# Kernel tuning notes

Measured on AMD Instinct MI355X. Metric: run time of the kernel, lower is better.

## Reference

```python
import jax, jax.numpy as jnp
import numpy as np


def setup_inputs() -> dict:
    key = jax.random.key(0)
    k1, k2 = jax.random.split(key)
    q_embed = jax.random.normal(k1, (1000, 1024), dtype=jnp.float32)      # (V, D)
    conv_feat = jax.random.normal(k2, (64, 1024, 800), dtype=jnp.float32)  # (B, D, T)
    return {"q_embed": q_embed, "conv_feat": conv_feat}


def reference(q_embed, conv_feat):
    # sim_scores: (B, V, T) = q_embed (V, D) @ conv_feat (B, D, T), no scaling
    sim_scores = jnp.einsum('vd,bdt->bvt', q_embed, conv_feat)
    attention_weights = jax.nn.softmax(sim_scores, axis=2)  # over T
    # context: (B, V, D) = weights (B, V, T) @ conv_feat^T (B, T, D)
    context_vector = jnp.einsum('bvt,bdt->bvd', attention_weights, conv_feat)
    return (context_vector, attention_weights)
```

## Files before the change

### kernel.cpp

```cpp
#include <hip/hip_runtime.h>
#include <hip/hip_bf16.h>

typedef short bf16x8 __attribute__((ext_vector_type(8)));
typedef float f32x4 __attribute__((ext_vector_type(4)));

#define NV 1000
#define ND 1024
#define NT 800
#define NB 64

__device__ inline unsigned short f32_bf16(float f) {
    unsigned u = __builtin_bit_cast(unsigned, f);
    return (unsigned short)((u + 0x7FFFu + ((u >> 16) & 1u)) >> 16);
}
__device__ inline void split_bf16(float f, unsigned short& h, unsigned short& l) {
    unsigned u = __builtin_bit_cast(unsigned, f);
    unsigned hb = (u + 0x7FFFu + ((u >> 16) & 1u)) >> 16;
    h = (unsigned short)hb;
    float hf = __builtin_bit_cast(float, hb << 16);
    float lf = f - hf;
    unsigned ul = __builtin_bit_cast(unsigned, lf);
    l = (unsigned short)((ul + 0x7FFFu + ((ul >> 16) & 1u)) >> 16);
}

__device__ inline void gload16(const void* g, void* l) {
    __builtin_amdgcn_global_load_lds(
        (const __attribute__((address_space(1))) unsigned int*)g,
        (__attribute__((address_space(3))) unsigned int*)l, 16, 0, 0);
}

__global__ __launch_bounds__(256) void prep_q(const float* __restrict__ Q,
                                              unsigned short* __restrict__ Qh,
                                              unsigned short* __restrict__ Ql) {
    int idx = blockIdx.x * 256 + threadIdx.x;
    int row = idx >> 8;
    int c4 = (idx & 255) << 2;
    float4 f = make_float4(0.f, 0.f, 0.f, 0.f);
    if (row < NV) f = *(const float4*)(Q + (size_t)row * ND + c4);
    unsigned short h0,h1,h2,h3,l0,l1,l2,l3;
    split_bf16(f.x,h0,l0); split_bf16(f.y,h1,l1);
    split_bf16(f.z,h2,l2); split_bf16(f.w,h3,l3);
    *(ushort4*)(Qh + (size_t)row * ND + c4) = make_ushort4(h0,h1,h2,h3);
    *(ushort4*)(Ql + (size_t)row * ND + c4) = make_ushort4(l0,l1,l2,l3);
}

__global__ __launch_bounds__(256) void prep_c(const float* __restrict__ C,
                                              unsigned short* __restrict__ Cth,
                                              unsigned short* __restrict__ Ctl) {
    const int dt = blockIdx.x;
    const int tt = blockIdx.y;
    const int b  = blockIdx.z;
    const int tid = threadIdx.x;
    __shared__ float T[64][33];
    const float* Cb = C + (size_t)b * ND * NT;
    const int d0 = dt * 64, t0 = tt * 32;
#pragma unroll
    for (int r = 0; r < 2; ++r) {
        int idx = r * 256 + tid;
        int row = idx >> 3;
        int c4 = (idx & 7) << 2;
        float4 f = *(const float4*)(Cb + (size_t)(d0 + row) * NT + t0 + c4);
        T[row][c4 + 0] = f.x; T[row][c4 + 1] = f.y;
        T[row][c4 + 2] = f.z; T[row][c4 + 3] = f.w;
    }
    __syncthreads();
#pragma unroll
    for (int r = 0; r < 2; ++r) {
        int idx = r * 256 + tid;
        int trow = idx >> 4;
        int dc = (idx & 15) << 2;
        unsigned short h[4], l[4];
#pragma unroll
        for (int j = 0; j < 4; ++j) split_bf16(T[dc + j][trow], h[j], l[j]);
        size_t o = ((size_t)b * NT + t0 + trow) * ND + d0 + dc;
        *(ushort4*)(Cth + o) = make_ushort4(h[0],h[1],h[2],h[3]);
        *(ushort4*)(Ctl + o) = make_ushort4(l[0],l[1],l[2],l[3]);
    }
}

__global__ __launch_bounds__(256) void gemm1_kernel(const unsigned short* __restrict__ Qh,
                                                    const unsigned short* __restrict__ Ql,
                                                    const unsigned short* __restrict__ Cth,
                                                    const unsigned short* __restrict__ Ctl,
                                                    float* __restrict__ S) {
    const int h = blockIdx.x;
    const int L = (h & 7) * 320 + (h >> 3);
    const int bm = L & 7;
    const int rest = L >> 3;
    const int bn = rest % 5;
    const int b  = rest / 5;

    const int tid = threadIdx.x;
    const int lane = tid & 63;
    const int w = tid >> 6;
    const int wr = w >> 1, wc = w & 1;

    __shared__ unsigned short Ah[128 * 32];
    __shared__ unsigned short Al[128 * 32];
    __shared__ unsigned short Bh[160 * 32];
    __shared__ unsigned short Bl[160 * 32];

    const int v0 = bm * 128, t0 = bn * 160;
    const unsigned short* Agh = Qh + (size_t)v0 * ND;
    const unsigned short* Agl = Ql + (size_t)v0 * ND;
    const unsigned short* Bgh = Cth + ((size_t)b * NT + t0) * ND;
    const unsigned short* Bgl = Ctl + ((size_t)b * NT + t0) * ND;

    f32x4 acc[4][5];
#pragma unroll
    for (int i = 0; i < 4; ++i)
#pragma unroll
        for (int j = 0; j < 5; ++j) acc[i][j] = (f32x4){0.f, 0.f, 0.f, 0.f};

    const int srow = lane >> 2;
    const int sslot = lane & 3;

    for (int k0 = 0; k0 < ND; k0 += 32) {
        for (int i = w; i < 8; i += 4) {
            int row = i * 16 + srow;
            int c = ((sslot ^ (row & 3)) << 3) + k0;
            gload16(Agh + (size_t)row * ND + c, Ah + i * 512);
            gload16(Agl + (size_t)row * ND + c, Al + i * 512);
        }
        for (int i = w; i < 10; i += 4) {
            int row = i * 16 + srow;
            int c = ((sslot ^ (row & 3)) << 3) + k0;
            gload16(Bgh + (size_t)row * ND + c, Bh + i * 512);
            gload16(Bgl + (size_t)row * ND + c, Bl + i * 512);
        }
        __syncthreads();

        const int g = lane >> 4, rl = lane & 15;
        const int sx = (g ^ (rl & 3)) << 4;
        bf16x8 ah[4], al[4], bh[5], bl[5];
#pragma unroll
        for (int mf = 0; mf < 4; ++mf) {
            int off = (wr * 64 + mf * 16 + rl) * 64 + sx;
            ah[mf] = *(const bf16x8*)((const char*)Ah + off);
            al[mf] = *(const bf16x8*)((const char*)Al + off);
        }
#pragma unroll
        for (int nf = 0; nf < 5; ++nf) {
            int off = (wc * 80 + nf * 16 + rl) * 64 + sx;
            bh[nf] = *(const bf16x8*)((const char*)Bh + off);
            bl[nf] = *(const bf16x8*)((const char*)Bl + off);
        }
#pragma unroll
        for (int mf = 0; mf < 4; ++mf)
#pragma unroll
            for (int nf = 0; nf < 5; ++nf) {
                acc[mf][nf] = __builtin_amdgcn_mfma_f32_16x16x32_bf16(ah[mf], bh[nf], acc[mf][nf], 0, 0, 0);
                acc[mf][nf] = __builtin_amdgcn_mfma_f32_16x16x32_bf16(ah[mf], bl[nf], acc[mf][nf], 0, 0, 0);
                acc[mf][nf] = __builtin_amdgcn_mfma_f32_16x16x32_bf16(al[mf], bh[nf], acc[mf][nf], 0, 0, 0);
            }
        __syncthreads();
    }

    float* Sb = S + (size_t)b * NV * NT;
    const int g = lane >> 4, rl = lane & 15;
#pragma unroll
    for (int mf = 0; mf < 4; ++mf) {
#pragma unroll
        for (int nf = 0; nf < 5; ++nf) {
#pragma unroll
            for (int r = 0; r < 4; ++r) {
                int v = v0 + wr * 64 + mf * 16 + g * 4 + r;
                int t = t0 + wc * 80 + nf * 16 + rl;
                if (v < NV) Sb[(size_t)v * NT + t] = acc[mf][nf][r];
            }
        }
    }
}

__global__ __launch_bounds__(256) void softmax_kernel(float* __restrict__ S) {
    const int row = blockIdx.x * 4 + (threadIdx.x >> 6);
    const int lane = threadIdx.x & 63;
    float* p = S + (size_t)row * NT;
    float v[13];
    float m = -INFINITY;
#pragma unroll
    for (int i = 0; i < 13; ++i) {
        int t = i * 64 + lane;
        v[i] = (t < NT) ? p[t] : -INFINITY;
        m = fmaxf(m, v[i]);
    }
#pragma unroll
    for (int off = 32; off; off >>= 1) m = fmaxf(m, __shfl_xor(m, off));
    float s = 0.f;
#pragma unroll
    for (int i = 0; i < 13; ++i) {
        int t = i * 64 + lane;
        float e = (t < NT) ? __expf(v[i] - m) : 0.f;
        v[i] = e;
        s += e;
    }
#pragma unroll
    for (int off = 32; off; off >>= 1) s += __shfl_xor(s, off);
    const float inv = 1.0f / s;
#pragma unroll
    for (int i = 0; i < 13; ++i) {
        int t = i * 64 + lane;
        if (t < NT) p[t] = v[i] * inv;
    }
}

__global__ __launch_bounds__(256) void gemm2_kernel(const float* __restrict__ W,
                                                    const float* __restrict__ C,
                                                    float* __restrict__ O) {
    const int h = blockIdx.x;
    const int L = (h & 7) * 512 + (h >> 3);
    const int bm = L & 7;
    const int bn = (L >> 3) & 7;
    const int b  = L >> 6;
    const int tid = threadIdx.x;
    const int lane = tid & 63;
    const int wid = tid >> 6;
    const int wr = wid >> 1;
    const int wc = wid & 1;

    __shared__ unsigned short As[128][40];
    __shared__ unsigned short Bs[128][40];

    const float* Wb = W + (size_t)b * NV * NT;
    const float* Cb = C + (size_t)b * ND * NT;
    const int v0 = bm * 128;
    const int d0 = bn * 128;

    f32x4 acc[4][4];
#pragma unroll
    for (int i = 0; i < 4; ++i)
#pragma unroll
        for (int j = 0; j < 4; ++j) acc[i][j] = (f32x4){0.f, 0.f, 0.f, 0.f};

    for (int k0 = 0; k0 < NT; k0 += 32) {
#pragma unroll
        for (int r = 0; r < 4; ++r) {
            int idx = r * 256 + tid;
            int row = idx >> 3;
            int kq  = (idx & 7) << 2;
            int v = v0 + row; if (v > NV - 1) v = NV - 1;
            const float4 f = *(const float4*)(Wb + (size_t)v * NT + k0 + kq);
            *(ushort4*)&As[row][kq] = make_ushort4(f32_bf16(f.x), f32_bf16(f.y), f32_bf16(f.z), f32_bf16(f.w));
        }
#pragma unroll
        for (int r = 0; r < 4; ++r) {
            int idx = r * 256 + tid;
            int row = idx >> 3;
            int kq  = (idx & 7) << 2;
            const float4 f = *(const float4*)(Cb + (size_t)(d0 + row) * NT + k0 + kq);
            *(ushort4*)&Bs[row][kq] = make_ushort4(f32_bf16(f.x), f32_bf16(f.y), f32_bf16(f.z), f32_bf16(f.w));
        }
        __syncthreads();

        bf16x8 a[4], bfr[4];
        const int kk = (lane >> 4) << 3;
#pragma unroll
        for (int mf = 0; mf < 4; ++mf) {
            int row = wr * 64 + mf * 16 + (lane & 15);
            a[mf] = *(const bf16x8*)&As[row][kk];
        }
#pragma unroll
        for (int nf = 0; nf < 4; ++nf) {
            int row = wc * 64 + nf * 16 + (lane & 15);
            bfr[nf] = *(const bf16x8*)&Bs[row][kk];
        }
#pragma unroll
        for (int mf = 0; mf < 4; ++mf)
#pragma unroll
            for (int nf = 0; nf < 4; ++nf)
                acc[mf][nf] = __builtin_amdgcn_mfma_f32_16x16x32_bf16(a[mf], bfr[nf], acc[mf][nf], 0, 0, 0);
        __syncthreads();
    }

    float* Ob = O + (size_t)b * NV * ND;
#pragma unroll
    for (int mf = 0; mf < 4; ++mf) {
#pragma unroll
        for (int nf = 0; nf < 4; ++nf) {
#pragma unroll
            for (int r = 0; r < 4; ++r) {
                int v = v0 + wr * 64 + mf * 16 + (lane >> 4) * 4 + r;
                int d = d0 + wc * 64 + nf * 16 + (lane & 15);
                if (v < NV) Ob[(size_t)v * ND + d] = acc[mf][nf][r];
            }
        }
    }
}

extern "C" void kernel_launch(void* const* d_in, const int* in_sizes, int n_in,
                              void* d_out, int out_size, void* d_ws, size_t ws_size,
                              hipStream_t stream) {
    const float* Q = (const float*)d_in[0];
    const float* C = (const float*)d_in[1];
    float* ctx = (float*)d_out;
    float* wts = ctx + (size_t)NB * NV * ND;

    unsigned short* Cth = (unsigned short*)ctx;
    unsigned short* Ctl = Cth + (size_t)NB * NT * ND;
    unsigned short* Qh  = Ctl + (size_t)NB * NT * ND;
    unsigned short* Ql  = Qh + (size_t)1024 * ND;

    prep_q<<<dim3(1024), 256, 0, stream>>>(Q, Qh, Ql);
    prep_c<<<dim3(16, 25, NB), 256, 0, stream>>>(C, Cth, Ctl);
    gemm1_kernel<<<dim3(2560), 256, 0, stream>>>(Qh, Ql, Cth, Ctl, wts);
    softmax_kernel<<<dim3(16000), 256, 0, stream>>>(wts);
    gemm2_kernel<<<dim3(4096), 256, 0, stream>>>(wts, C, ctx);
}
```

Before: 798.7 us.

## Pre-convert softmax weights and conv features to bf16 for direct-load gemm2

Softmax now also writes a bf16 copy of the attention weights, and prep_c writes a bf16 copy of conv_feat in its original layout, both into workspace. A new gemm2 path loads these bf16 tiles straight into swizzled shared memory with 16-byte loads, so it no longer reads fp32 and converts inside the GEMM. There are fallback variants for when the workspace is too small. The cost is extra global writes of two large bf16 buffers in earlier kernels, and the path depends on ws_size.

Result: faster. 735.6 us (-7.9%).

```diff
diff --git a/kernel.cpp b/kernel.cpp
--- a/kernel.cpp
+++ b/kernel.cpp
@@ -46,7 +46,9 @@
 
 __global__ __launch_bounds__(256) void prep_c(const float* __restrict__ C,
                                               unsigned short* __restrict__ Cth,
-                                              unsigned short* __restrict__ Ctl) {
+                                              unsigned short* __restrict__ Ctl,
+                                              unsigned short* __restrict__ Cbf,
+                                              int writeCbf) {
     const int dt = blockIdx.x;
     const int tt = blockIdx.y;
     const int b  = blockIdx.z;
@@ -62,6 +64,10 @@
         float4 f = *(const float4*)(Cb + (size_t)(d0 + row) * NT + t0 + c4);
         T[row][c4 + 0] = f.x; T[row][c4 + 1] = f.y;
         T[row][c4 + 2] = f.z; T[row][c4 + 3] = f.w;
+        if (writeCbf) {
+            *(ushort4*)(Cbf + ((size_t)b * ND + d0 + row) * NT + t0 + c4) =
+                make_ushort4(f32_bf16(f.x), f32_bf16(f.y), f32_bf16(f.z), f32_bf16(f.w));
+        }
     }
     __syncthreads();
 #pragma unroll
@@ -172,10 +178,13 @@
     }
 }
 
-__global__ __launch_bounds__(256) void softmax_kernel(float* __restrict__ S) {
+__global__ __launch_bounds__(256) void softmax_kernel(float* __restrict__ S,
+                                                      unsigned short* __restrict__ Wbf,
+                                                      int writeWbf) {
     const int row = blockIdx.x * 4 + (threadIdx.x >> 6);
     const int lane = threadIdx.x & 63;
     float* p = S + (size_t)row * NT;
+    unsigned short* pw = Wbf + (size_t)row * NT;
     float v[13];
     float m = -INFINITY;
 #pragma unroll
@@ -200,13 +209,177 @@
 #pragma unroll
     for (int i = 0; i < 13; ++i) {
         int t = i * 64 + lane;
-        if (t < NT) p[t] = v[i] * inv;
-    }
-}
-
-__global__ __launch_bounds__(256) void gemm2_kernel(const float* __restrict__ W,
-                                                    const float* __restrict__ C,
-                                                    float* __restrict__ O) {
+        if (t < NT) {
+            float wv = v[i] * inv;
+            p[t] = wv;
+            if (writeWbf) pw[t] = f32_bf16(wv);
+        }
+    }
+}
+
+__global__ __launch_bounds__(256) void gemm2_fast(const unsigned short* __restrict__ Wbf,
+                                                  const unsigned short* __restrict__ Cbf,
+                                                  float* __restrict__ O) {
+    const int h = blockIdx.x;
+    const int L = (h & 7) * 512 + (h >> 3);
+    const int bm = L & 7;
+    const int bn = (L >> 3) & 7;
+    const int b  = L >> 6;
+    const int tid = threadIdx.x;
+    const int lane = tid & 63;
+    const int w = tid >> 6;
+    const int wr = w >> 1, wc = w & 1;
+
+    __shared__ unsigned short As[128 * 32];
+    __shared__ unsigned short Bs[128 * 32];
+
+    const int v0 = bm * 128, d0 = bn * 128;
+    const unsigned short* Ag = Wbf + (size_t)b * NV * NT;
+    const unsigned short* Bg = Cbf + ((size_t)b * ND + d0) * NT;
+
+    f32x4 acc[4][4];
+#pragma unroll
+    for (int i = 0; i < 4; ++i)
+#pragma unroll
+        for (int j = 0; j < 4; ++j) acc[i][j] = (f32x4){0.f, 0.f, 0.f, 0.f};
+
+    const int srow = lane >> 2;
+    const int sslot = lane & 3;
+
+    for (int k0 = 0; k0 < NT; k0 += 32) {
+        for (int i = w; i < 8; i += 4) {
+            int row = i * 16 + srow;
+            int c = ((sslot ^ (row & 3)) << 3) + k0;
+            int vrow = v0 + row; if (vrow > NV - 1) vrow = NV - 1;
+            gload16(Ag + (size_t)vrow * NT + c, As + i * 512);
+            gload16(Bg + (size_t)row * NT + c, Bs + i * 512);
+        }
+        __syncthreads();
+
+        const int g = lane >> 4, rl = lane & 15;
+        const int sx = (g ^ (rl & 3)) << 4;
+        bf16x8 a[4], bfr[4];
+#pragma unroll
+        for (int mf = 0; mf < 4; ++mf) {
+            int off = (wr * 64 + mf * 16 + rl) * 64 + sx;
+            a[mf] = *(const bf16x8*)((const char*)As + off);
+        }
+#pragma unroll
+        for (int nf = 0; nf < 4; ++nf) {
+            int off = (wc * 64 + nf * 16 + rl) * 64 + sx;
+            bfr[nf] = *(const bf16x8*)((const char*)Bs + off);
+        }
+#pragma unroll
+        for (int mf = 0; mf < 4; ++mf)
+#pragma unroll
+            for (int nf = 0; nf < 4; ++nf)
+                acc[mf][nf] = __builtin_amdgcn_mfma_f32_16x16x32_bf16(a[mf], bfr[nf], acc[mf][nf], 0, 0, 0);
+        __syncthreads();
+    }
+
+    float* Ob = O + (size_t)b * NV * ND;
+    const int g = lane >> 4, rl = lane & 15;
+#pragma unroll
+    for (int mf = 0; mf < 4; ++mf) {
+#pragma unroll
+        for (int nf = 0; nf < 4; ++nf) {
+#pragma unroll
+            for (int r = 0; r < 4; ++r) {
+                int v = v0 + wr * 64 + mf * 16 + g * 4 + r;
+                int d = d0 + wc * 64 + nf * 16 + rl;
+                if (v < NV) Ob[(size_t)v * ND + d] = acc[mf][nf][r];
+            }
+        }
+    }
+}
+
+__global__ __launch_bounds__(256) void gemm2_mid(const unsigned short* __restrict__ Wbf,
+                                                 const float* __restrict__ C,
+                                                 float* __restrict__ O) {
+    const int h = blockIdx.x;
+    const int L = (h & 7) * 512 + (h >> 3);
+    const int bm = L & 7;
+    const int bn = (L >> 3) & 7;
+    const int b  = L >> 6;
+    const int tid = threadIdx.x;
+    const int lane = tid & 63;
+    const int w = tid >> 6;
+    const int wr = w >> 1, wc = w & 1;
+
+    __shared__ unsigned short As[128 * 32];
+    __shared__ unsigned short Bs[128][40];
+
+    const int v0 = bm * 128, d0 = bn * 128;
+    const unsigned short* Ag = Wbf + (size_t)b * NV * NT;
+    const float* Cb = C + (size_t)b * ND * NT;
+
+    f32x4 acc[4][4];
+#pragma unroll
+    for (int i = 0; i < 4; ++i)
+#pragma unroll
+        for (int j = 0; j < 4; ++j) acc[i][j] = (f32x4){0.f, 0.f, 0.f, 0.f};
+
+    const int srow = lane >> 2;
+    const int sslot = lane & 3;
+
+    for (int k0 = 0; k0 < NT; k0 += 32) {
+        for (int i = w; i < 8; i += 4) {
+            int row = i * 16 + srow;
+            int c = ((sslot ^ (row & 3)) << 3) + k0;
+            int vrow = v0 + row; if (vrow > NV - 1) vrow = NV - 1;
+            gload16(Ag + (size_t)vrow * NT + c, As + i * 512);
+        }
+#pragma unroll
+        for (int r = 0; r < 4; ++r) {
+            int idx = r * 256 + tid;
+            int row = idx >> 3;
+            int kq  = (idx & 7) << 2;
+            const float4 f = *(const float4*)(Cb + (size_t)(d0 + row) * NT + k0 + kq);
+            *(ushort4*)&Bs[row][kq] = make_ushort4(f32_bf16(f.x), f32_bf16(f.y), f32_bf16(f.z), f32_bf16(f.w));
+        }
+        __syncthreads();
+
+        const int g = lane >> 4, rl = lane & 15;
+        const int sx = (g ^ (rl & 3)) << 4;
+        const int kk = g << 3;
+        bf16x8 a[4], bfr[4];
+#pragma unroll
+        for (int mf = 0; mf < 4; ++mf) {
+            int off = (wr * 64 + mf * 16 + rl) * 64 + sx;
+            a[mf] = *(const bf16x8*)((const char*)As + off);
+        }
+#pragma unroll
+        for (int nf = 0; nf < 4; ++nf) {
+            int row = wc * 64 + nf * 16 + rl;
+            bfr[nf] = *(const bf16x8*)&Bs[row][kk];
+        }
+#pragma unroll
+        for (int mf = 0; mf < 4; ++mf)
+#pragma unroll
+            for (int nf = 0; nf < 4; ++nf)
+                acc[mf][nf] = __builtin_amdgcn_mfma_f32_16x16x32_bf16(a[mf], bfr[nf], acc[mf][nf], 0, 0, 0);
+        __syncthreads();
+    }
+
+    float* Ob = O + (size_t)b * NV * ND;
+    const int g = lane >> 4, rl = lane & 15;
+#pragma unroll
+    for (int mf = 0; mf < 4; ++mf) {
+#pragma unroll
+        for (int nf = 0; nf < 4; ++nf) {
+#pragma unroll
+            for (int r = 0; r < 4; ++r) {
+                int v = v0 + wr * 64 + mf * 16 + g * 4 + r;
+                int d = d0 + wc * 64 + nf * 16 + rl;
+                if (v < NV) Ob[(size_t)v * ND + d] = acc[mf][nf][r];
+            }
+        }
+    }
+}
+
+__global__ __launch_bounds__(256) void gemm2_slow(const float* __restrict__ W,
+                                                  const float* __restrict__ C,
+                                                  float* __restrict__ O) {
     const int h = blockIdx.x;
     const int L = (h & 7) * 512 + (h >> 3);
     const int bm = L & 7;
@@ -300,9 +473,18 @@
     unsigned short* Qh  = Ctl + (size_t)NB * NT * ND;
     unsigned short* Ql  = Qh + (size_t)1024 * ND;
 
+    const size_t WbfBytes = (size_t)NB * NV * NT * 2;
+    const size_t CbfBytes = (size_t)NB * ND * NT * 2;
+    unsigned short* Wbf = (unsigned short*)d_ws;
+    unsigned short* Cbf = (unsigned short*)((char*)d_ws + WbfBytes);
+    const int wsFast = ws_size >= WbfBytes + CbfBytes;
+    const int wsMid  = ws_size >= WbfBytes;
+
     prep_q<<<dim3(1024), 256, 0, stream>>>(Q, Qh, Ql);
-    prep_c<<<dim3(16, 25, NB), 256, 0, stream>>>(C, Cth, Ctl);
+    prep_c<<<dim3(16, 25, NB), 256, 0, stream>>>(C, Cth, Ctl, Cbf, wsFast);
     gemm1_kernel<<<dim3(2560), 256, 0, stream>>>(Qh, Ql, Cth, Ctl, wts);
-    softmax_kernel<<<dim3(16000), 256, 0, stream>>>(wts);
-    gemm2_kernel<<<dim3(4096), 256, 0, stream>>>(wts, C, ctx);
-}
+    softmax_kernel<<<dim3(16000), 256, 0, stream>>>(wts, Wbf, wsMid);
+    if (wsFast)      gemm2_fast<<<dim3(4096), 256, 0, stream>>>(Wbf, Cbf, ctx);
+    else if (wsMid)  gemm2_mid<<<dim3(4096), 256, 0, stream>>>(Wbf, C, ctx);
+    else             gemm2_slow<<<dim3(4096), 256, 0, stream>>>(wts, C, ctx);
+}
```
